# Performance work log

Hardware: AMD Instinct MI355X
Metric: run time of the kernel (lower is better)

The kernel has to match this reference:

```python
import jax, jax.numpy as jnp
import numpy as np

N_NODES = 8192
N_EDGES = 262144
D_IN = 512
D_OUT = 512


def setup_inputs() -> dict:
    key = jax.random.key(0)
    k1, k2, k3 = jax.random.split(key, 3)
    x = jax.random.normal(k1, (N_NODES, D_IN), dtype=jnp.float32)
    edge_index = jax.random.randint(k2, (2, N_EDGES), 0, N_NODES, dtype=jnp.int64)
    weight = jax.random.normal(k3, (D_IN, D_OUT), dtype=jnp.float32)
    bias = jnp.zeros((D_OUT,), dtype=jnp.float32)
    return {"x": x, "edge_index": edge_index, "weight": weight, "bias": bias}


def reference(x, edge_index, weight, bias):
    # GCN layer with selfloop=True branch of the original module.
    n = x.shape[0]
    # Dense symmetric adjacency via scatter-set, matching adj[ei0,ei1]=1; adj[ei1,ei0]=1
    adj = jnp.zeros((n, n), dtype=x.dtype)
    adj = adj.at[edge_index[0], edge_index[1]].set(1.0)
    adj = adj.at[edge_index[1], edge_index[0]].set(1.0)
    # Add self loops, symmetric degree normalization D^{-1/2} A D^{-1/2}
    adj = adj + jnp.eye(n, dtype=x.dtype)
    deg = jnp.sum(adj, axis=1)
    dinv = 1.0 / jnp.sqrt(deg)
    adj = adj * dinv[:, None] * dinv[None, :]  # == D @ adj @ D (diagonal scaling)
    return adj @ (x @ weight) + bias
```

## Files before the change

kernel.cpp:

```cpp
#include <hip/hip_runtime.h>
#include <hip/hip_bf16.h>


#define ELL_STRIDE 128

typedef __attribute__((ext_vector_type(8))) short bf16x8;
typedef __attribute__((ext_vector_type(4))) float f32x4;

__device__ __forceinline__ unsigned short f2bf(float f) {
  unsigned u = __float_as_uint(f);
  u = (u + 0x7fff + ((u >> 16) & 1)) >> 16;
  return (unsigned short)u;
}
__device__ __forceinline__ float bflo(unsigned u) {
  return __uint_as_float(u << 16);
}
__device__ __forceinline__ float bfhi(unsigned u) {
  return __uint_as_float(u & 0xffff0000u);
}

__global__ __launch_bounds__(256) void build_adj_kernel(
    const int* __restrict__ ei, unsigned* __restrict__ mask,
    int n_edges, int words) {
  int e = blockIdx.x * blockDim.x + threadIdx.x;
  if (e >= n_edges) return;
  int u = ei[e];
  int v = ei[e + n_edges];
  atomicOr(&mask[(size_t)u * words + (v >> 5)], 1u << (v & 31));
  atomicOr(&mask[(size_t)v * words + (u >> 5)], 1u << (u & 31));
}

__global__ __launch_bounds__(256) void build_ell_kernel(
    const unsigned* __restrict__ mask, unsigned short* __restrict__ ell,
    int* __restrict__ deg, float* __restrict__ dinv, int n, int words) {
  int gtid = blockIdx.x * blockDim.x + threadIdx.x;
  int node = gtid >> 6;
  int lane = threadIdx.x & 63;
  if (node >= n) return;
  const unsigned* __restrict__ row = mask + (size_t)node * words;
  unsigned short* __restrict__ out = ell + (size_t)node * ELL_STRIDE;

  int running = 0;
  for (int r = 0; r < words; r += 64) {
    const int w = r + lane;
    unsigned bits = row[w];
    const int cnt = __popc(bits);
    int x = cnt;
#pragma unroll
    for (int d = 1; d < 64; d <<= 1) {
      int y = __shfl_up(x, d, 64);
      if (lane >= d) x += y;
    }
    int pos = running + x - cnt;
    while (bits) {
      const int b = __builtin_ctz(bits);
      bits &= bits - 1;
      if (pos < ELL_STRIDE) out[pos] = (unsigned short)((w << 5) + b);
      ++pos;
    }
    running += __shfl(x, 63, 64);
  }
  if (lane == 0) {
    deg[node] = running < ELL_STRIDE ? running : ELL_STRIDE;
    dinv[node] = rsqrtf((float)running + 1.0f);
  }
}

__global__ __launch_bounds__(256) void cast_bf16_kernel(
    const float* __restrict__ in, unsigned short* __restrict__ out, int n4) {
  int t = blockIdx.x * blockDim.x + threadIdx.x;
  if (t >= n4) return;
  float4 v = ((const float4*)in)[t];
  ushort4 o;
  o.x = f2bf(v.x); o.y = f2bf(v.y); o.z = f2bf(v.z); o.w = f2bf(v.w);
  ((ushort4*)out)[t] = o;
}

__global__ __launch_bounds__(256) void transpose_cast_kernel(
    const float* __restrict__ W, unsigned short* __restrict__ Wt, int K, int N) {
  __shared__ float tile[32][33];
  const int tx = threadIdx.x & 31;
  const int ty = threadIdx.x >> 5;
  const int bx = blockIdx.x, by = blockIdx.y;
#pragma unroll
  for (int r = 0; r < 4; ++r)
    tile[ty + 8 * r][tx] = W[(size_t)(by * 32 + ty + 8 * r) * N + bx * 32 + tx];
  __syncthreads();
#pragma unroll
  for (int r = 0; r < 4; ++r)
    Wt[(size_t)(bx * 32 + ty + 8 * r) * K + by * 32 + tx] =
        f2bf(tile[tx][ty + 8 * r]);
}

__global__ __launch_bounds__(256) void gemm_mfma_kernel(
    const unsigned short* __restrict__ xb,
    const unsigned short* __restrict__ Wt,
    const float* __restrict__ dinv,
    unsigned short* __restrict__ Hs,
    int M, int N, int K) {
  __shared__ unsigned short As[512 * 8];
  __shared__ unsigned short Bs[512 * 8];

  const int tid = threadIdx.x;
  const int wave = tid >> 6;
  const int lane = tid & 63;
  const int q = lane >> 4;
  const int c = lane & 15;
  const int m0 = blockIdx.y * 128;
  const int n0 = blockIdx.x * 128;
  const int wr = wave >> 1, wc = wave & 1;

  f32x4 acc[4][4] = {};

  for (int k0 = 0; k0 < K; k0 += 32) {
#pragma unroll
    for (int t = 0; t < 2; ++t) {
      const int sbase = wave * 128 + t * 64;
      const int s = sbase + lane;
      const int kc = s >> 7, row = s & 127;
      const unsigned short* g = xb + (size_t)(m0 + row) * K + k0 + kc * 8;
      __builtin_amdgcn_global_load_lds(
          (const __attribute__((address_space(1))) void*)g,
          (__attribute__((address_space(3))) void*)(As + sbase * 8), 16, 0, 0);
    }
#pragma unroll
    for (int t = 0; t < 2; ++t) {
      const int sbase = wave * 128 + t * 64;
      const int s = sbase + lane;
      const int n = s >> 2, kc = s & 3;
      const unsigned short* g = Wt + (size_t)(n0 + n) * K + k0 + kc * 8;
      __builtin_amdgcn_global_load_lds(
          (const __attribute__((address_space(1))) void*)g,
          (__attribute__((address_space(3))) void*)(Bs + sbase * 8), 16, 0, 0);
    }
    __syncthreads();

    bf16x8 a[4], b[4];
#pragma unroll
    for (int tm = 0; tm < 4; ++tm) {
      const int row = wr * 64 + tm * 16 + c;
      a[tm] = *(const bf16x8*)(As + (q * 128 + row) * 8);
    }
#pragma unroll
    for (int tn = 0; tn < 4; ++tn) {
      const int n = wc * 64 + tn * 16 + c;
      b[tn] = *(const bf16x8*)(Bs + (n * 4 + q) * 8);
    }
#pragma unroll
    for (int tm = 0; tm < 4; ++tm)
#pragma unroll
      for (int tn = 0; tn < 4; ++tn)
        acc[tm][tn] = __builtin_amdgcn_mfma_f32_16x16x32_bf16(
            a[tm], b[tn], acc[tm][tn], 0, 0, 0);
    __syncthreads();
  }

#pragma unroll
  for (int tm = 0; tm < 4; ++tm) {
#pragma unroll
    for (int r = 0; r < 4; ++r) {
      const int grow = m0 + wr * 64 + tm * 16 + q * 4 + r;
      const float di = dinv[grow];
#pragma unroll
      for (int tn = 0; tn < 4; ++tn) {
        const int gcol = n0 + wc * 64 + tn * 16 + c;
        Hs[(size_t)grow * N + gcol] = f2bf(di * acc[tm][tn][r]);
      }
    }
  }
}

__global__ __launch_bounds__(256) void spmm_kernel(
    const unsigned short* __restrict__ ell, const int* __restrict__ deg,
    const unsigned short* __restrict__ Hs, const float* __restrict__ dinv,
    const float* __restrict__ bias, float* __restrict__ out, int n, int D) {
  __shared__ unsigned short jl[4][ELL_STRIDE];
  const int wave = threadIdx.x >> 6, lane = threadIdx.x & 63;
  const int i = blockIdx.x * 4 + wave;

  jl[wave][lane] = ell[(size_t)i * ELL_STRIDE + lane];
  jl[wave][64 + lane] = ell[(size_t)i * ELL_STRIDE + 64 + lane];
  const int d = deg[i];

  const unsigned short* __restrict__ hb = Hs + lane * 8;
  float acc[8] = {0.f, 0.f, 0.f, 0.f, 0.f, 0.f, 0.f, 0.f};
#pragma unroll 8
  for (int k = 0; k < d; ++k) {
    const int j = jl[wave][k];
    const uint4 h = *(const uint4*)(hb + (size_t)j * D);
    acc[0] += bflo(h.x); acc[1] += bfhi(h.x);
    acc[2] += bflo(h.y); acc[3] += bfhi(h.y);
    acc[4] += bflo(h.z); acc[5] += bfhi(h.z);
    acc[6] += bflo(h.w); acc[7] += bfhi(h.w);
  }

  const uint4 hs = *(const uint4*)(hb + (size_t)i * D);
  acc[0] += bflo(hs.x); acc[1] += bfhi(hs.x);
  acc[2] += bflo(hs.y); acc[3] += bfhi(hs.y);
  acc[4] += bflo(hs.z); acc[5] += bfhi(hs.z);
  acc[6] += bflo(hs.w); acc[7] += bfhi(hs.w);

  const float di = dinv[i];
  const float4 b0 = *(const float4*)(bias + lane * 8);
  const float4 b1 = *(const float4*)(bias + lane * 8 + 4);
  float4 o0, o1;
  o0.x = di * acc[0] + b0.x; o0.y = di * acc[1] + b0.y;
  o0.z = di * acc[2] + b0.z; o0.w = di * acc[3] + b0.w;
  o1.x = di * acc[4] + b1.x; o1.y = di * acc[5] + b1.y;
  o1.z = di * acc[6] + b1.z; o1.w = di * acc[7] + b1.w;
  *(float4*)(out + (size_t)i * D + lane * 8) = o0;
  *(float4*)(out + (size_t)i * D + lane * 8 + 4) = o1;
}

extern "C" void kernel_launch(void* const* d_in, const int* in_sizes, int n_in,
                              void* d_out, int out_size, void* d_ws, size_t ws_size,
                              hipStream_t stream) {
  const float* x    = (const float*)d_in[0];
  const int*   ei   = (const int*)d_in[1];
  const float* W    = (const float*)d_in[2];
  const float* bias = (const float*)d_in[3];
  float* out = (float*)d_out;

  const int d_out_dim = in_sizes[3];
  const int d_in_dim  = in_sizes[2] / d_out_dim;
  const int n_nodes   = in_sizes[0] / d_in_dim;
  const int n_edges   = in_sizes[1] / 2;
  const int words     = (n_nodes + 31) / 32;

  char* ws = (char*)d_ws;
  size_t off = 0;
  unsigned* mask = (unsigned*)(ws + off); off += (size_t)n_nodes * words * 4;
  float* dinv    = (float*)(ws + off);    off += (size_t)n_nodes * 4;
  int* deg       = (int*)(ws + off);      off += (size_t)n_nodes * 4;
  unsigned short* ell = (unsigned short*)(ws + off); off += (size_t)n_nodes * ELL_STRIDE * 2;
  unsigned short* xb  = (unsigned short*)(ws + off); off += (size_t)n_nodes * d_in_dim * 2;
  unsigned short* Wt  = (unsigned short*)(ws + off); off += (size_t)d_in_dim * d_out_dim * 2;
  unsigned short* Hs  = (unsigned short*)(ws + off); off += (size_t)n_nodes * d_out_dim * 2;

  hipMemsetAsync(mask, 0, (size_t)n_nodes * words * sizeof(unsigned), stream);

  build_adj_kernel<<<(n_edges + 255) / 256, 256, 0, stream>>>(ei, mask, n_edges, words);

  build_ell_kernel<<<(n_nodes * 64 + 255) / 256, 256, 0, stream>>>(mask, ell, deg, dinv,
                                                                   n_nodes, words);

  const int n4 = n_nodes * d_in_dim / 4;
  cast_bf16_kernel<<<(n4 + 255) / 256, 256, 0, stream>>>(x, xb, n4);

  dim3 tgrid(d_out_dim / 32, d_in_dim / 32);
  transpose_cast_kernel<<<tgrid, 256, 0, stream>>>(W, Wt, d_in_dim, d_out_dim);

  dim3 ggrid(d_out_dim / 128, n_nodes / 128);
  gemm_mfma_kernel<<<ggrid, 256, 0, stream>>>(xb, Wt, dinv, Hs,
                                              n_nodes, d_out_dim, d_in_dim);

  spmm_kernel<<<n_nodes / 4, 256, 0, stream>>>(ell, deg, Hs, dinv, bias, out,
                                               n_nodes, d_out_dim);
}
```

Baseline: 163.4 us.

## Fuse edge scatter, x cast and W transpose into one launch; shrink GEMM tiles

Merges the adjacency atomicOr scatter, the x fp32-to-bf16 cast and the W transpose-cast into a single kernel that dispatches on block index, removing two launches and letting these independent jobs overlap. The GEMM tile shrinks from 128x128 to 64x64, giving 1024 blocks instead of 256 so more of the GPU's compute units have work. Smaller tiles reduce data reuse per block and raise global/LDS traffic per FLOP. The fused kernel's transpose blocks also allocate shared memory that the other block types do not need.

```diff
diff --git a/kernel.cpp b/kernel.cpp
--- a/kernel.cpp
+++ b/kernel.cpp
@@ -19,15 +19,49 @@
   return __uint_as_float(u & 0xffff0000u);
 }
 
-__global__ __launch_bounds__(256) void build_adj_kernel(
-    const int* __restrict__ ei, unsigned* __restrict__ mask,
-    int n_edges, int words) {
-  int e = blockIdx.x * blockDim.x + threadIdx.x;
-  if (e >= n_edges) return;
-  int u = ei[e];
-  int v = ei[e + n_edges];
-  atomicOr(&mask[(size_t)u * words + (v >> 5)], 1u << (v & 31));
-  atomicOr(&mask[(size_t)v * words + (u >> 5)], 1u << (u & 31));
+__global__ __launch_bounds__(256) void fused_front_kernel(
+    const int* __restrict__ ei, unsigned* __restrict__ mask, int n_edges,
+    int words,
+    const float* __restrict__ x, unsigned short* __restrict__ xb, int n4,
+    const float* __restrict__ W, unsigned short* __restrict__ Wt, int K, int N,
+    int edge_blocks, int cast_blocks) {
+  const int bid = blockIdx.x;
+  if (bid < edge_blocks) {
+    const int e = bid * 256 + threadIdx.x;
+    if (e < n_edges) {
+      const int u = ei[e];
+      const int v = ei[e + n_edges];
+      atomicOr(&mask[(size_t)u * words + (v >> 5)], 1u << (v & 31));
+      atomicOr(&mask[(size_t)v * words + (u >> 5)], 1u << (u & 31));
+    }
+    return;
+  }
+  if (bid < edge_blocks + cast_blocks) {
+    const int t = (bid - edge_blocks) * 256 + threadIdx.x;
+    if (t < n4) {
+      float4 v = ((const float4*)x)[t];
+      ushort4 o;
+      o.x = f2bf(v.x); o.y = f2bf(v.y); o.z = f2bf(v.z); o.w = f2bf(v.w);
+      ((ushort4*)xb)[t] = o;
+    }
+    return;
+  }
+  {
+    __shared__ float tile[32][33];
+    const int b = bid - edge_blocks - cast_blocks;
+    const int bx = b & ((N >> 5) - 1);
+    const int by = b >> (31 - __builtin_clz(N >> 5));
+    const int tx = threadIdx.x & 31;
+    const int ty = threadIdx.x >> 5;
+#pragma unroll
+    for (int r = 0; r < 4; ++r)
+      tile[ty + 8 * r][tx] = W[(size_t)(by * 32 + ty + 8 * r) * N + bx * 32 + tx];
+    __syncthreads();
+#pragma unroll
+    for (int r = 0; r < 4; ++r)
+      Wt[(size_t)(bx * 32 + ty + 8 * r) * K + by * 32 + tx] =
+          f2bf(tile[tx][ty + 8 * r]);
+  }
 }
 
 __global__ __launch_bounds__(256) void build_ell_kernel(
@@ -66,104 +100,72 @@
   }
 }
 
-__global__ __launch_bounds__(256) void cast_bf16_kernel(
-    const float* __restrict__ in, unsigned short* __restrict__ out, int n4) {
-  int t = blockIdx.x * blockDim.x + threadIdx.x;
-  if (t >= n4) return;
-  float4 v = ((const float4*)in)[t];
-  ushort4 o;
-  o.x = f2bf(v.x); o.y = f2bf(v.y); o.z = f2bf(v.z); o.w = f2bf(v.w);
-  ((ushort4*)out)[t] = o;
-}
-
-__global__ __launch_bounds__(256) void transpose_cast_kernel(
-    const float* __restrict__ W, unsigned short* __restrict__ Wt, int K, int N) {
-  __shared__ float tile[32][33];
-  const int tx = threadIdx.x & 31;
-  const int ty = threadIdx.x >> 5;
-  const int bx = blockIdx.x, by = blockIdx.y;
-#pragma unroll
-  for (int r = 0; r < 4; ++r)
-    tile[ty + 8 * r][tx] = W[(size_t)(by * 32 + ty + 8 * r) * N + bx * 32 + tx];
-  __syncthreads();
-#pragma unroll
-  for (int r = 0; r < 4; ++r)
-    Wt[(size_t)(bx * 32 + ty + 8 * r) * K + by * 32 + tx] =
-        f2bf(tile[tx][ty + 8 * r]);
-}
-
 __global__ __launch_bounds__(256) void gemm_mfma_kernel(
     const unsigned short* __restrict__ xb,
     const unsigned short* __restrict__ Wt,
     const float* __restrict__ dinv,
     unsigned short* __restrict__ Hs,
     int M, int N, int K) {
-  __shared__ unsigned short As[512 * 8];
-  __shared__ unsigned short Bs[512 * 8];
+  __shared__ unsigned short As[256 * 8];
+  __shared__ unsigned short Bs[256 * 8];
 
   const int tid = threadIdx.x;
   const int wave = tid >> 6;
   const int lane = tid & 63;
   const int q = lane >> 4;
   const int c = lane & 15;
-  const int m0 = blockIdx.y * 128;
-  const int n0 = blockIdx.x * 128;
+  const int m0 = blockIdx.y * 64;
+  const int n0 = blockIdx.x * 64;
   const int wr = wave >> 1, wc = wave & 1;
 
-  f32x4 acc[4][4] = {};
+  f32x4 acc[2][2] = {};
 
   for (int k0 = 0; k0 < K; k0 += 32) {
-#pragma unroll
-    for (int t = 0; t < 2; ++t) {
-      const int sbase = wave * 128 + t * 64;
-      const int s = sbase + lane;
-      const int kc = s >> 7, row = s & 127;
-      const unsigned short* g = xb + (size_t)(m0 + row) * K + k0 + kc * 8;
+    {
+      const int s = tid;
+      const unsigned short* g = xb + (size_t)(m0 + (s & 63)) * K + k0 + (s >> 6) * 8;
       __builtin_amdgcn_global_load_lds(
           (const __attribute__((address_space(1))) void*)g,
-          (__attribute__((address_space(3))) void*)(As + sbase * 8), 16, 0, 0);
-    }
-#pragma unroll
-    for (int t = 0; t < 2; ++t) {
-      const int sbase = wave * 128 + t * 64;
-      const int s = sbase + lane;
-      const int n = s >> 2, kc = s & 3;
-      const unsigned short* g = Wt + (size_t)(n0 + n) * K + k0 + kc * 8;
+          (__attribute__((address_space(3))) void*)(As + wave * 64 * 8), 16, 0, 0);
+    }
+    {
+      const int s = tid;
+      const unsigned short* g = Wt + (size_t)(n0 + (s >> 2)) * K + k0 + (s & 3) * 8;
       __builtin_amdgcn_global_load_lds(
           (const __attribute__((address_space(1))) void*)g,
-          (__attribute__((address_space(3))) void*)(Bs + sbase * 8), 16, 0, 0);
+          (__attribute__((address_space(3))) void*)(Bs + wave * 64 * 8), 16, 0, 0);
     }
     __syncthreads();
 
-    bf16x8 a[4], b[4];
-#pragma unroll
-    for (int tm = 0; tm < 4; ++tm) {
-      const int row = wr * 64 + tm * 16 + c;
-      a[tm] = *(const bf16x8*)(As + (q * 128 + row) * 8);
-    }
-#pragma unroll
-    for (int tn = 0; tn < 4; ++tn) {
-      const int n = wc * 64 + tn * 16 + c;
+    bf16x8 a[2], b[2];
+#pragma unroll
+    for (int tm = 0; tm < 2; ++tm) {
+      const int row = wr * 32 + tm * 16 + c;
+      a[tm] = *(const bf16x8*)(As + (q * 64 + row) * 8);
+    }
+#pragma unroll
+    for (int tn = 0; tn < 2; ++tn) {
+      const int n = wc * 32 + tn * 16 + c;
       b[tn] = *(const bf16x8*)(Bs + (n * 4 + q) * 8);
     }
 #pragma unroll
-    for (int tm = 0; tm < 4; ++tm)
-#pragma unroll
-      for (int tn = 0; tn < 4; ++tn)
+    for (int tm = 0; tm < 2; ++tm)
+#pragma unroll
+      for (int tn = 0; tn < 2; ++tn)
         acc[tm][tn] = __builtin_amdgcn_mfma_f32_16x16x32_bf16(
             a[tm], b[tn], acc[tm][tn], 0, 0, 0);
     __syncthreads();
   }
 
 #pragma unroll
-  for (int tm = 0; tm < 4; ++tm) {
+  for (int tm = 0; tm < 2; ++tm) {
 #pragma unroll
     for (int r = 0; r < 4; ++r) {
-      const int grow = m0 + wr * 64 + tm * 16 + q * 4 + r;
+      const int grow = m0 + wr * 32 + tm * 16 + q * 4 + r;
       const float di = dinv[grow];
 #pragma unroll
-      for (int tn = 0; tn < 4; ++tn) {
-        const int gcol = n0 + wc * 64 + tn * 16 + c;
+      for (int tn = 0; tn < 2; ++tn) {
+        const int gcol = n0 + wc * 32 + tn * 16 + c;
         Hs[(size_t)grow * N + gcol] = f2bf(di * acc[tm][tn][r]);
       }
     }
@@ -239,18 +241,18 @@
 
   hipMemsetAsync(mask, 0, (size_t)n_nodes * words * sizeof(unsigned), stream);
 
-  build_adj_kernel<<<(n_edges + 255) / 256, 256, 0, stream>>>(ei, mask, n_edges, words);
-
-  build_ell_kernel<<<(n_nodes * 64 + 255) / 256, 256, 0, stream>>>(mask, ell, deg, dinv,
-                                                                   n_nodes, words);
-
+  const int edge_blocks = (n_edges + 255) / 256;
   const int n4 = n_nodes * d_in_dim / 4;
-  cast_bf16_kernel<<<(n4 + 255) / 256, 256, 0, stream>>>(x, xb, n4);
-
-  dim3 tgrid(d_out_dim / 32, d_in_dim / 32);
-  transpose_cast_kernel<<<tgrid, 256, 0, stream>>>(W, Wt, d_in_dim, d_out_dim);
-
-  dim3 ggrid(d_out_dim / 128, n_nodes / 128);
+  const int cast_blocks = (n4 + 255) / 256;
+  const int tr_blocks = (d_in_dim / 32) * (d_out_dim / 32);
+  fused_front_kernel<<<edge_blocks + cast_blocks + tr_blocks, 256, 0, stream>>>(
+      ei, mask, n_edges, words, x, xb, n4, W, Wt, d_in_dim, d_out_dim,
+      edge_blocks, cast_blocks);
+
+  build_ell_kernel<<<(n_nodes * 64 + 255) / 256, 256, 0, stream>>>(
+      mask, ell, deg, dinv, n_nodes, words);
+
+  dim3 ggrid(d_out_dim / 64, n_nodes / 64);
   gemm_mfma_kernel<<<ggrid, 256, 0, stream>>>(xb, Wt, dinv, Hs,
                                               n_nodes, d_out_dim, d_in_dim);
 
```

Result: faster. 158.3 us (-3.1%).
